# Kernel tuning notes

Measured on AMD Instinct MI355X. Metric: run time of the kernel, lower is better.

## Reference

```python
import jax, jax.numpy as jnp
import numpy as np

E = 512   # embed_size
H = 512   # hidden_size
V = 32000 # vocab_size
B = 32
P = 196   # num_pixels
T = 32    # seq_len


def setup_inputs() -> dict:
    key = jax.random.key(0)
    ks = jax.random.split(key, 16)
    s = 0.02
    return {
        "features": jax.random.normal(ks[0], (B, P, E), dtype=jnp.float32),
        "captions": jax.random.randint(ks[1], (B, T), 0, V),
        "embed_W": jax.random.normal(ks[2], (V, E), dtype=jnp.float32) * s,
        "attn_W": jax.random.normal(ks[3], (H, E + H), dtype=jnp.float32) * s,
        "attn_b": jnp.zeros((H,), dtype=jnp.float32),
        "v_w": jax.random.normal(ks[4], (H,), dtype=jnp.float32) * s,
        "W_ih": jax.random.normal(ks[5], (4 * H, 2 * E), dtype=jnp.float32) * s,
        "W_hh": jax.random.normal(ks[6], (4 * H, H), dtype=jnp.float32) * s,
        "b_ih": jnp.zeros((4 * H,), dtype=jnp.float32),
        "b_hh": jnp.zeros((4 * H,), dtype=jnp.float32),
        "lin_W": jax.random.normal(ks[7], (V, H), dtype=jnp.float32) * s,
        "lin_b": jnp.zeros((V,), dtype=jnp.float32),
        "inith_W": jax.random.normal(ks[8], (H, E), dtype=jnp.float32) * s,
        "inith_b": jnp.zeros((H,), dtype=jnp.float32),
        "initc_W": jax.random.normal(ks[9], (H, E), dtype=jnp.float32) * s,
        "initc_b": jnp.zeros((H,), dtype=jnp.float32),
    }


def _decode(features, captions, embed_W, attn_W, attn_b, v_w,
            W_ih, W_hh, b_ih, b_hh, lin_W, lin_b,
            inith_W, inith_b, initc_W, initc_b):
    mean_feat = features.mean(axis=1)                       # [B,E]
    h0 = mean_feat @ inith_W.T + inith_b                    # [B,H]
    c0 = mean_feat @ initc_W.T + initc_b                    # [B,H]
    emb = embed_W[captions]                                  # [B,T,E]

    # split attention weight: attn(cat(features, hidden)) = feat@Wf.T + h@Wh.T + b
    Wf = attn_W[:, :E]                                       # [H,E]
    Wh = attn_W[:, E:]                                       # [H,H]
    # features are constant across timesteps: project once
    feat_proj = jnp.einsum('bpe,he->bph', features, Wf)      # [B,P,H]

    def step(carry, x_t):
        h, c = carry
        # Bahdanau attention
        energy = jnp.tanh(feat_proj + (h @ Wh.T)[:, None, :] + attn_b)  # [B,P,H]
        scores = jnp.einsum('bph,h->bp', energy, v_w)                    # [B,P]
        alpha = jax.nn.softmax(scores, axis=1)
        context = jnp.einsum('bp,bpe->be', alpha, features)              # [B,E]
        # LSTM cell (PyTorch gate order i,f,g,o)
        x = jnp.concatenate([x_t, context], axis=-1)                     # [B,2E]
        gates = x @ W_ih.T + b_ih + h @ W_hh.T + b_hh                    # [B,4H]
        i, f, g, o = jnp.split(gates, 4, axis=-1)
        c_new = jax.nn.sigmoid(f) * c + jax.nn.sigmoid(i) * jnp.tanh(g)
        h_new = jax.nn.sigmoid(o) * jnp.tanh(c_new)
        logits = h_new @ lin_W.T + lin_b                                 # [B,V]
        return (h_new, c_new), logits

    xs = jnp.transpose(emb, (1, 0, 2))                        # [T,B,E]
    _, outs = jax.lax.scan(step, (h0, c0), xs)                # [T,B,V]
    return jnp.transpose(outs, (1, 0, 2))                     # [B,T,V]


def reference(features, captions, embed_W, attn_W, attn_b, v_w,
              W_ih, W_hh, b_ih, b_hh, lin_W, lin_b,
              inith_W, inith_b, initc_W, initc_b):
    return _decode(features, captions, embed_W, attn_W, attn_b, v_w,
                   W_ih, W_hh, b_ih, b_hh, lin_W, lin_b,
                   inith_W, inith_b, initc_W, initc_b)
```

## Files before the change

kernel.cpp:

```cpp
#include <hip/hip_runtime.h>

#define E 512
#define H 512
#define V 32000
#define B 32
#define P 196
#define T 32
#define NB 256
#define NT 512

typedef __attribute__((ext_vector_type(8))) short s8v;
typedef __attribute__((ext_vector_type(4))) float f4v;

__device__ __forceinline__ float bf16_to_f(unsigned short u){
  return __uint_as_float(((unsigned)u) << 16);
}
__device__ __forceinline__ unsigned short f_to_bf16(float f){
  unsigned u = __float_as_uint(f);
  u += 0x7FFFu + ((u >> 16) & 1u);
  return (unsigned short)(u >> 16);
}
__device__ __forceinline__ float fast_tanh(float x){
  float e = __expf(2.0f*x);
  return 1.0f - 2.0f/(e + 1.0f);
}
__device__ __forceinline__ float sigmoidf_(float x){
  return 1.0f/(1.0f + __expf(-x));
}
__device__ __forceinline__ void load_lds16(const unsigned short* g, unsigned short* l){
  __builtin_amdgcn_global_load_lds(
      (const __attribute__((address_space(1))) void*)g,
      (__attribute__((address_space(3))) void*)l, 16, 0, 0);
}
__device__ __forceinline__ float dot4(float4 a, float4 b){
  return a.x*b.x + a.y*b.y + a.z*b.z + a.w*b.w;
}

#define AT_SCOPE __HIP_MEMORY_SCOPE_AGENT
__device__ __forceinline__ void cohstore(float* p, float v){
  __hip_atomic_store(p, v, __ATOMIC_RELAXED, AT_SCOPE);
}
__device__ __forceinline__ unsigned cohldu(const unsigned* p){
  return __hip_atomic_load(p, __ATOMIC_RELAXED, AT_SCOPE);
}
__device__ __forceinline__ void cohstu(unsigned* p, unsigned v){
  __hip_atomic_store(p, v, __ATOMIC_RELAXED, AT_SCOPE);
}

__device__ __forceinline__ void bar_arrive(unsigned* my, unsigned gen){
  __syncthreads();
  if (threadIdx.x == 0) cohstu(my, gen);
}
__device__ __forceinline__ void bar_wait(const unsigned* base, unsigned gen){
  if (threadIdx.x < 64){
    for (;;){
      unsigned mn = 0xffffffffu;
      for (int i = (int)threadIdx.x; i < 8; i += 64){
        unsigned v = cohldu(base + i);
        mn = v < mn ? v : mn;
      }
      #pragma unroll
      for (int off = 32; off; off >>= 1){
        unsigned o2 = (unsigned)__shfl_xor((int)mn, off);
        mn = o2 < mn ? o2 : mn;
      }
      if (mn >= gen) break;
      __builtin_amdgcn_s_sleep(1);
    }
    __builtin_amdgcn_sched_barrier(0);
  }
  __syncthreads();
}

__global__ void split_kernel(const float* __restrict__ src, int src_ld, int src_coff,
                             int rows,
                             unsigned short* __restrict__ dhi, unsigned short* __restrict__ dlo,
                             int dst_ld, int dst_coff)
{
  int n = rows << 9;
  for (int i = blockIdx.x*blockDim.x + threadIdx.x; i < n; i += gridDim.x*blockDim.x){
    int r = i >> 9, c = i & 511;
    float x = src[(size_t)r*src_ld + src_coff + c];
    unsigned short h = f_to_bf16(x);
    dhi[(size_t)r*dst_ld + dst_coff + c] = h;
    if (dlo) dlo[(size_t)r*dst_ld + dst_coff + c] = f_to_bf16(x - bf16_to_f(h));
  }
}

__global__ void embed_kernel(const int* __restrict__ caps, const float* __restrict__ embW,
                             unsigned short* __restrict__ ehi, unsigned short* __restrict__ elo)
{
  int row = blockIdx.x;
  int cap = caps[row];
  const float* s = embW + (size_t)cap*E;
  for (int e = threadIdx.x; e < E; e += blockDim.x){
    float x = s[e];
    unsigned short h = f_to_bf16(x);
    ehi[(size_t)row*E + e] = h;
    elo[(size_t)row*E + e] = f_to_bf16(x - bf16_to_f(h));
  }
}

__global__ __launch_bounds__(512) void prep_kernel(
    const float* __restrict__ feats,
    const float* __restrict__ inith_W, const float* __restrict__ inith_b,
    const float* __restrict__ initc_W, const float* __restrict__ initc_b,
    float* __restrict__ hgrp, float* __restrict__ c_state)
{
  __shared__ float mf[E];
  const int b = blockIdx.x, tid = threadIdx.x;
  const float* fb = feats + (size_t)b*P*E + tid;
  float s = 0.f;
  for (int p = 0; p < P; ++p) s += fb[(size_t)p*E];
  mf[tid] = s * (1.0f/196.0f);
  __syncthreads();
  const float* wh = inith_W + (size_t)tid*E;
  const float* wc = initc_W + (size_t)tid*E;
  float h0 = inith_b[tid], c0 = initc_b[tid];
  #pragma unroll 4
  for (int e = 0; e < E; e += 4){
    float4 a4 = *(const float4*)(wh + e);
    float4 b4 = *(const float4*)(wc + e);
    float4 m4 = *(const float4*)(mf + e);
    h0 += dot4(a4, m4);
    c0 += dot4(b4, m4);
  }
  hgrp[(size_t)b*512 + tid] = h0;
  c_state[b*512 + tid] = c0;
}

__global__ __launch_bounds__(256) void transpose_wh_kernel(
    const float* __restrict__ attn_W, float* __restrict__ WhT)
{
  __shared__ float tile[64][65];
  const int jt = blockIdx.x & 7, kt = blockIdx.x >> 3;
  const int tx = threadIdx.x & 63, ty = threadIdx.x >> 6;
  for (int r = ty; r < 64; r += 4)
    tile[r][tx] = attn_W[(size_t)(jt*64 + r)*(E+H) + E + kt*64 + tx];
  __syncthreads();
  for (int r = ty; r < 64; r += 4)
    WhT[(size_t)(kt*64 + r)*512 + jt*64 + tx] = tile[tx][r];
}

__global__ __launch_bounds__(256) void pack_whh_kernel(
    const float* __restrict__ Whh, float* __restrict__ Wpackh)
{
  __shared__ float tile[64][65];
  const int sub = blockIdx.x & 7, cg = (blockIdx.x >> 3) & 3, kg = blockIdx.x >> 5;
  const int tx = threadIdx.x & 63, ty = threadIdx.x >> 6;
  const int kbase = kg*64;
  for (int cl = ty; cl < 64; cl += 4){
    const int c = cg*64 + cl;
    const int gcol = (c >> 6)*512 + sub*64 + (c & 63);
    tile[cl][tx] = Whh[(size_t)gcol*512 + kbase + tx];
  }
  __syncthreads();
  for (int kk = ty; kk < 64; kk += 4)
    Wpackh[((size_t)sub*512 + kbase + kk)*256 + cg*64 + tx] = tile[tx][kk];
}

__global__ __launch_bounds__(256) void gemm_bt_kernel(
    const unsigned short* __restrict__ A0, const unsigned short* __restrict__ A1,
    const unsigned short* __restrict__ A2,
    const unsigned short* __restrict__ B0, const unsigned short* __restrict__ B1,
    const unsigned short* __restrict__ B2,
    float* __restrict__ Cc, const float* __restrict__ bias,
    int N, int K, int npasses, int mt, int swz)
{
  __shared__ __align__(16) unsigned short Al[128*32];
  __shared__ __align__(16) unsigned short Bl[128*32];
  const int tid = threadIdx.x;
  const int wid = tid >> 6, l = tid & 63;
  int f = blockIdx.x;
  if (swz) f = (f & 7)*((int)gridDim.x >> 3) + (f >> 3);
  const int m0 = (f % mt)*128, n0 = (f / mt)*128;
  const int wr = wid >> 1, wc = wid & 1;

  f4v acc[4][4];
  #pragma unroll
  for (int i = 0; i < 4; ++i)
    #pragma unroll
    for (int j = 0; j < 4; ++j) acc[i][j] = (f4v){0.f,0.f,0.f,0.f};

  const int s0 = tid, s1 = tid + 256;
  const int r0 = s0 >> 2, g0 = (s0 & 3) ^ ((r0 >> 1) & 3);
  const int r1 = s1 >> 2, g1 = (s1 & 3) ^ ((r1 >> 1) & 3);
  const int la = l & 15, ch = l >> 4;

  for (int pass = 0; pass < npasses; ++pass){
    const unsigned short* Ap = pass == 0 ? A0 : (pass == 1 ? A1 : A2);
    const unsigned short* Bp = pass == 0 ? B0 : (pass == 1 ? B1 : B2);
    for (int k0 = 0; k0 < K; k0 += 32){
      __syncthreads();
      load_lds16(Ap + (size_t)(m0 + r0)*K + k0 + g0*8, Al + s0*8);
      load_lds16(Ap + (size_t)(m0 + r1)*K + k0 + g1*8, Al + s1*8);
      load_lds16(Bp + (size_t)(n0 + r0)*K + k0 + g0*8, Bl + s0*8);
      load_lds16(Bp + (size_t)(n0 + r1)*K + k0 + g1*8, Bl + s1*8);
      __syncthreads();
      s8v av[4], bv[4];
      #pragma unroll
      for (int mi = 0; mi < 4; ++mi){
        int row = wr*64 + mi*16 + la;
        int cs = ch ^ ((row >> 1) & 3);
        av[mi] = *(const s8v*)(Al + (row*4 + cs)*8);
      }
      #pragma unroll
      for (int ni = 0; ni < 4; ++ni){
        int row = wc*64 + ni*16 + la;
        int cs = ch ^ ((row >> 1) & 3);
        bv[ni] = *(const s8v*)(Bl + (row*4 + cs)*8);
      }
      #pragma unroll
      for (int mi = 0; mi < 4; ++mi)
        #pragma unroll
        for (int ni = 0; ni < 4; ++ni)
          acc[mi][ni] = __builtin_amdgcn_mfma_f32_16x16x32_bf16(av[mi], bv[ni], acc[mi][ni], 0, 0, 0);
    }
  }
  #pragma unroll
  for (int mi = 0; mi < 4; ++mi){
    int row = m0 + wr*64 + mi*16 + (l >> 4)*4;
    #pragma unroll
    for (int ni = 0; ni < 4; ++ni){
      int col = n0 + wc*64 + ni*16 + (l & 15);
      float bb = bias ? bias[col] : 0.0f;
      #pragma unroll
      for (int r = 0; r < 4; ++r)
        Cc[(size_t)(row + r)*N + col] = acc[mi][ni][r] + bb;
    }
  }
}

__global__ __launch_bounds__(512, 1) void loop_kernel(
    const float* __restrict__ feat_proj,
    const float* __restrict__ WhT, const float* __restrict__ attn_b,
    const float* __restrict__ v_w, const float* __restrict__ Wpackh,
    const float* __restrict__ FW, const float* __restrict__ gates_emb,
    const float* __restrict__ b_ih, const float* __restrict__ b_hh,
    float* __restrict__ hgrp,
    const float* __restrict__ c_init,
    float* __restrict__ sps,
    unsigned short* __restrict__ hall_h, unsigned short* __restrict__ hall_l,
    unsigned* __restrict__ fm1, unsigned* __restrict__ fm3)
{
  __shared__ float hs[512];
  __shared__ float hwl[64];
  __shared__ float partA[8][72];
  __shared__ float aux[256];
  __shared__ float biasl[256];
  __shared__ float red[512];
  __shared__ float smx, sinv;

  const int blk = blockIdx.x, tid = threadIdx.x;
  const int b = blk >> 3, sub = blk & 7;
  const int gbase = blk & ~7;
  const int l = tid & 63, wv = tid >> 6;

  float wreg[64];
  #pragma unroll
  for (int kk = 0; kk < 64; ++kk)
    wreg[kk] = WhT[(size_t)(wv*64 + kk)*512 + sub*64 + l];
  float fpreg[25];
  #pragma unroll
  for (int i = 0; i < 25; ++i){
    const int p = wv + i*8;
    fpreg[i] = (p < P) ? feat_proj[((size_t)b*P + p)*512 + sub*64 + l] : 0.f;
  }
  for (int c = tid; c < 256; c += NT){
    const int gcol = (c >> 6)*512 + sub*64 + (c & 63);
    biasl[c] = b_ih[gcol] + b_hh[gcol];
  }
  const float vl = v_w[sub*64 + l];
  const float ab = (tid < 64) ? attn_b[sub*64 + tid] : 0.f;
  float c_reg = 0.f;
  if (tid < 64) c_reg = c_init[b*512 + sub*64 + tid];

  const int dc = tid & 255;
  const int kh = tid >> 8;
  const int gcol_d = (dc >> 6)*512 + sub*64 + (dc & 63);
  const float* wp_h = Wpackh + ((size_t)sub*512 + kh*256)*256 + dc;
  __syncthreads();

  for (int t = 0; t < T; ++t){
    const unsigned gen = (unsigned)(t + 1);

    float gepre[4];
    if (tid < 64){
      const float* ge = gates_emb + ((size_t)b*T + t)*2048;
      #pragma unroll
      for (int g = 0; g < 4; ++g) gepre[g] = ge[g*512 + sub*64 + tid];
    }

    hs[tid] = hgrp[((size_t)t*B + b)*512 + tid];
    __syncthreads();
    {
      const float* hk = hs + wv*64;
      float a = 0.f;
      #pragma unroll
      for (int kk = 0; kk < 64; ++kk) a += hk[kk] * wreg[kk];
      partA[wv][l] = a;
    }
    __syncthreads();
    if (tid < 64){
      float s = ab;
      #pragma unroll
      for (int k = 0; k < 8; ++k) s += partA[k][tid];
      hwl[tid] = s;
    }
    __syncthreads();

    {
      const float hj = hwl[l];
      float* spw = sps + (size_t)(t*B + b)*1600 + sub;
      #pragma unroll
      for (int i = 0; i < 25; ++i){
        const int p = wv + i*8;
        if (p >= P) break;
        float e2 = vl * fast_tanh(fpreg[i] + hj);
        #pragma unroll
        for (int off = 32; off; off >>= 1) e2 += __shfl_xor(e2, off);
        if (l == 0) cohstore(spw + p*8, e2);
      }
    }
    bar_arrive(fm1 + blk, gen);

    float acch0 = 0.f, acch1 = 0.f, acch2 = 0.f, acch3 = 0.f;
    {
      const float* hk = hs + kh*256;
      #pragma unroll 8
      for (int k = 0; k < 256; k += 4){
        acch0 += wp_h[(size_t)(k+0)*256] * hk[k+0];
        acch1 += wp_h[(size_t)(k+1)*256] * hk[k+1];
        acch2 += wp_h[(size_t)(k+2)*256] * hk[k+2];
        acch3 += wp_h[(size_t)(k+3)*256] * hk[k+3];
      }
    }
    bar_wait(fm1 + gbase, gen);

    {
      float sc_v = -1e30f;
      if (tid < P){
        const float* sp = sps + (size_t)(t*B + b)*1600 + tid*8;
        float4 q0 = *(const float4*)sp, q1 = *(const float4*)(sp + 4);
        sc_v = (q0.x + q0.y + q0.z + q0.w) + (q1.x + q1.y + q1.z + q1.w);
      }
      if (tid < 256) aux[tid] = sc_v;
      __syncthreads();
      if (tid < 64){
        float m = -1e30f;
        #pragma unroll
        for (int i = 0; i < 4; ++i) m = fmaxf(m, aux[tid + i*64]);
        #pragma unroll
        for (int off = 32; off; off >>= 1) m = fmaxf(m, __shfl_xor(m, off));
        if (tid == 0) smx = m;
      }
      __syncthreads();
      float al = (tid < P) ? __expf(sc_v - smx) : 0.f;
      if (tid < 256) aux[tid] = al;
      __syncthreads();
      if (tid < 64){
        float s = 0.f;
        #pragma unroll
        for (int i = 0; i < 4; ++i) s += aux[tid + i*64];
        #pragma unroll
        for (int off = 32; off; off >>= 1) s += __shfl_xor(s, off);
        if (tid == 0) sinv = 1.0f/s;
      }
      __syncthreads();
    }

    float accc = 0.f;
    {
      const float* fwb = FW + ((size_t)b*P + kh*98)*2048 + gcol_d;
      const float* ax = aux + kh*98;
      #pragma unroll 7
      for (int i = 0; i < 98; ++i)
        accc += ax[i] * fwb[(size_t)i*2048];
    }
    red[dc*2 + kh] = ((acch0 + acch1) + (acch2 + acch3)) + accc*sinv;
    __syncthreads();

    if (tid < 64){
      float gv[4];
      #pragma unroll
      for (int g = 0; g < 4; ++g){
        const int c = g*64 + tid;
        gv[g] = red[c*2] + red[c*2 + 1] + biasl[c] + gepre[g];
      }
      const float i_ = sigmoidf_(gv[0]);
      const float f_ = sigmoidf_(gv[1]);
      const float g_ = fast_tanh(gv[2]);
      const float o_ = sigmoidf_(gv[3]);
      const int j = sub*64 + tid;
      const float c_new = f_*c_reg + i_*g_;
      const float h_new = o_*fast_tanh(c_new);
      c_reg = c_new;
      cohstore(hgrp + ((size_t)(t+1)*B + b)*512 + j, h_new);
      const unsigned short hh = f_to_bf16(h_new);
      aux[tid] = __uint_as_float(((unsigned)hh << 16) |
                 (unsigned)f_to_bf16(h_new - bf16_to_f(hh)));
    }
    bar_arrive(fm3 + blk, gen);
    if (tid < 64){
      const unsigned pk = __float_as_uint(aux[tid]);
      const int j = sub*64 + tid;
      hall_h[((size_t)b*T + t)*512 + j] = (unsigned short)(pk >> 16);
      hall_l[((size_t)b*T + t)*512 + j] = (unsigned short)(pk & 0xffffu);
    }
    bar_wait(fm3 + gbase, gen);
  }
}

extern "C" void kernel_launch(void* const* d_in, const int* in_sizes, int n_in,
                              void* d_out, int out_size, void* d_ws, size_t ws_size,
                              hipStream_t stream)
{
  (void)in_sizes; (void)n_in; (void)out_size;
  const float* features = (const float*)d_in[0];
  const int*   captions = (const int*)d_in[1];
  const float* embed_W  = (const float*)d_in[2];
  const float* attn_W   = (const float*)d_in[3];
  const float* attn_b   = (const float*)d_in[4];
  const float* v_w      = (const float*)d_in[5];
  const float* W_ih     = (const float*)d_in[6];
  const float* W_hh     = (const float*)d_in[7];
  const float* b_ih     = (const float*)d_in[8];
  const float* b_hh     = (const float*)d_in[9];
  const float* lin_W    = (const float*)d_in[10];
  const float* lin_b    = (const float*)d_in[11];
  const float* inith_W  = (const float*)d_in[12];
  const float* inith_b  = (const float*)d_in[13];
  const float* initc_W  = (const float*)d_in[14];
  const float* initc_b  = (const float*)d_in[15];

  char* o = (char*)d_out;
  unsigned short* feat_hi   = (unsigned short*)o; o += (size_t)(B*P)*E*2;
  unsigned short* feat_lo   = (unsigned short*)o; o += (size_t)(B*P)*E*2;
  unsigned short* Wf_bf     = (unsigned short*)o; o += (size_t)H*E*2;
  float*          feat_proj = (float*)o;          o += (size_t)(B*P)*H*4;
  unsigned short* emb_hi    = (unsigned short*)o; o += (size_t)(B*T)*E*2;
  unsigned short* emb_lo    = (unsigned short*)o; o += (size_t)(B*T)*E*2;
  unsigned short* Wihe_hi   = (unsigned short*)o; o += (size_t)2048*512*2;
  unsigned short* Wihe_lo   = (unsigned short*)o; o += (size_t)2048*512*2;
  unsigned short* Wihc_hi   = (unsigned short*)o; o += (size_t)2048*512*2;
  unsigned short* Wihc_lo   = (unsigned short*)o; o += (size_t)2048*512*2;
  float*          gates_emb = (float*)o;          o += (size_t)(B*T)*2048*4;
  float*          Wpackh    = (float*)o;          o += (size_t)8*512*256*4;
  float*          FW        = (float*)o;          o += (size_t)(B*P)*2048*4;

  const size_t SZ_LIN  = (size_t)V*H*2;
  const size_t SZ_HALL = (size_t)(B*T)*H*2;
  const size_t SZ_HG   = (size_t)(T+1)*B*512*4;
  const size_t SZ_SPS  = (size_t)T*B*200*8*4;
  const size_t SZ_ST   = (size_t)B*H*4;
  const size_t SZ_WHT  = (size_t)H*H*4;
  const size_t SZ_FLG  = 4096;
  const size_t need_wo = SZ_LIN + 2*SZ_HALL + SZ_HG + SZ_SPS + SZ_ST + SZ_WHT + SZ_FLG;
  const bool three = (ws_size >= need_wo + SZ_LIN);

  char* w = (char*)d_ws;
  unsigned short* lin_hi  = (unsigned short*)w; w += SZ_LIN;
  unsigned short* lin_lo  = (unsigned short*)w; if (three) w += SZ_LIN;
  unsigned short* hall_hi = (unsigned short*)w; w += SZ_HALL;
  unsigned short* hall_lo = (unsigned short*)w; w += SZ_HALL;
  float*          hgrp    = (float*)w;          w += SZ_HG;
  float*          sps     = (float*)w;          w += SZ_SPS;
  float*          c_state = (float*)w;          w += SZ_ST;
  float*          WhT_ws  = (float*)w;          w += SZ_WHT;
  unsigned*       flags   = (unsigned*)w;       w += SZ_FLG;
  unsigned* fm1 = flags;
  unsigned* fm3 = flags + 256;

  split_kernel<<<2048, 256, 0, stream>>>(features, E, 0, B*P, feat_hi, feat_lo, E, 0);
  split_kernel<<<256, 256, 0, stream>>>(attn_W, E+H, 0, H, Wf_bf, nullptr, E, 0);
  split_kernel<<<2048, 256, 0, stream>>>(lin_W, 512, 0, V, lin_hi, three ? lin_lo : nullptr, 512, 0);
  split_kernel<<<1024, 256, 0, stream>>>(W_ih, 1024, 0, 2048, Wihe_hi, Wihe_lo, 512, 0);
  split_kernel<<<1024, 256, 0, stream>>>(W_ih, 1024, 512, 2048, Wihc_hi, Wihc_lo, 512, 0);
  embed_kernel<<<B*T, 256, 0, stream>>>(captions, embed_W, emb_hi, emb_lo);
  prep_kernel<<<B, 512, 0, stream>>>(features, inith_W, inith_b, initc_W, initc_b,
                                     hgrp, c_state);
  transpose_wh_kernel<<<64, 256, 0, stream>>>(attn_W, WhT_ws);
  pack_whh_kernel<<<256, 256, 0, stream>>>(W_hh, Wpackh);
  hipMemsetAsync(flags, 0, SZ_FLG, stream);

  gemm_bt_kernel<<<(B*P/128)*(E/128), 256, 0, stream>>>(
      feat_hi, feat_hi, feat_hi, Wf_bf, Wf_bf, Wf_bf,
      feat_proj, nullptr, E, E, 1, B*P/128, 0);
  gemm_bt_kernel<<<(B*T/128)*(2048/128), 256, 0, stream>>>(
      emb_hi, emb_lo, emb_hi, Wihe_hi, Wihe_hi, Wihe_lo,
      gates_emb, nullptr, 2048, 512, 3, B*T/128, 1);
  gemm_bt_kernel<<<(B*P/128)*(2048/128), 256, 0, stream>>>(
      feat_hi, feat_lo, feat_hi, Wihc_hi, Wihc_hi, Wihc_lo,
      FW, nullptr, 2048, 512, 3, B*P/128, 1);

  loop_kernel<<<NB, NT, 0, stream>>>(
      feat_proj, WhT_ws, attn_b, v_w, Wpackh, FW, gates_emb, b_ih, b_hh,
      hgrp, c_state, sps, hall_hi, hall_lo, fm1, fm3);

  gemm_bt_kernel<<<(V/128)*(B*T/128), 256, 0, stream>>>(
      hall_hi, hall_lo, hall_hi, lin_hi, lin_hi, three ? lin_lo : lin_hi,
      (float*)d_out, lin_b, V, H, three ? 3 : 2, B*T/128, 1);
}
```

Before: 1.061 ms.

## Store W_hh pack in bf16 and remap blocks so subs interleave across batches

The packed recurrent weight W_hh used in the per-step LSTM gate dot products is now stored as bf16 instead of fp32, halving the bytes streamed each timestep. Block-to-(batch,sub) mapping changes from b=blk>>3 to b=blk&31 so that blocks sharing the same weight slice are adjacent, which may improve L2 locality across CUs/XCDs. Flag indices are recomputed to match the new mapping. This lowers the precision of the h@W_hh product, which could affect accuracy.

After: 1.029 ms. -2.9%, faster.

```diff
diff --git a/kernel.cpp b/kernel.cpp
--- a/kernel.cpp
+++ b/kernel.cpp
@@ -143,7 +143,7 @@
 }
 
 __global__ __launch_bounds__(256) void pack_whh_kernel(
-    const float* __restrict__ Whh, float* __restrict__ Wpackh)
+    const float* __restrict__ Whh, unsigned short* __restrict__ Wpackh)
 {
   __shared__ float tile[64][65];
   const int sub = blockIdx.x & 7, cg = (blockIdx.x >> 3) & 3, kg = blockIdx.x >> 5;
@@ -156,7 +156,7 @@
   }
   __syncthreads();
   for (int kk = ty; kk < 64; kk += 4)
-    Wpackh[((size_t)sub*512 + kbase + kk)*256 + cg*64 + tx] = tile[tx][kk];
+    Wpackh[((size_t)sub*512 + kbase + kk)*256 + cg*64 + tx] = f_to_bf16(tile[tx][kk]);
 }
 
 __global__ __launch_bounds__(256) void gemm_bt_kernel(
@@ -234,7 +234,7 @@
 __global__ __launch_bounds__(512, 1) void loop_kernel(
     const float* __restrict__ feat_proj,
     const float* __restrict__ WhT, const float* __restrict__ attn_b,
-    const float* __restrict__ v_w, const float* __restrict__ Wpackh,
+    const float* __restrict__ v_w, const unsigned short* __restrict__ Wpackh,
     const float* __restrict__ FW, const float* __restrict__ gates_emb,
     const float* __restrict__ b_ih, const float* __restrict__ b_hh,
     float* __restrict__ hgrp,
@@ -252,8 +252,7 @@
   __shared__ float smx, sinv;
 
   const int blk = blockIdx.x, tid = threadIdx.x;
-  const int b = blk >> 3, sub = blk & 7;
-  const int gbase = blk & ~7;
+  const int b = blk & 31, sub = blk >> 5;
   const int l = tid & 63, wv = tid >> 6;
 
   float wreg[64];
@@ -278,7 +277,8 @@
   const int dc = tid & 255;
   const int kh = tid >> 8;
   const int gcol_d = (dc >> 6)*512 + sub*64 + (dc & 63);
-  const float* wp_h = Wpackh + ((size_t)sub*512 + kh*256)*256 + dc;
+  const unsigned short* wp_h = Wpackh + ((size_t)sub*512 + kh*256)*256 + dc;
+  const float* fw_th = FW + ((size_t)b*P + kh*98)*2048 + gcol_d;
   __syncthreads();
 
   for (int t = 0; t < T; ++t){
@@ -322,20 +322,20 @@
         if (l == 0) cohstore(spw + p*8, e2);
       }
     }
-    bar_arrive(fm1 + blk, gen);
+    bar_arrive(fm1 + b*8 + sub, gen);
 
     float acch0 = 0.f, acch1 = 0.f, acch2 = 0.f, acch3 = 0.f;
     {
       const float* hk = hs + kh*256;
       #pragma unroll 8
       for (int k = 0; k < 256; k += 4){
-        acch0 += wp_h[(size_t)(k+0)*256] * hk[k+0];
-        acch1 += wp_h[(size_t)(k+1)*256] * hk[k+1];
-        acch2 += wp_h[(size_t)(k+2)*256] * hk[k+2];
-        acch3 += wp_h[(size_t)(k+3)*256] * hk[k+3];
-      }
-    }
-    bar_wait(fm1 + gbase, gen);
+        acch0 += bf16_to_f(wp_h[(size_t)(k+0)*256]) * hk[k+0];
+        acch1 += bf16_to_f(wp_h[(size_t)(k+1)*256]) * hk[k+1];
+        acch2 += bf16_to_f(wp_h[(size_t)(k+2)*256]) * hk[k+2];
+        acch3 += bf16_to_f(wp_h[(size_t)(k+3)*256]) * hk[k+3];
+      }
+    }
+    bar_wait(fm1 + b*8, gen);
 
     {
       float sc_v = -1e30f;
@@ -371,11 +371,10 @@
 
     float accc = 0.f;
     {
-      const float* fwb = FW + ((size_t)b*P + kh*98)*2048 + gcol_d;
       const float* ax = aux + kh*98;
       #pragma unroll 7
       for (int i = 0; i < 98; ++i)
-        accc += ax[i] * fwb[(size_t)i*2048];
+        accc += ax[i] * fw_th[(size_t)i*2048];
     }
     red[dc*2 + kh] = ((acch0 + acch1) + (acch2 + acch3)) + accc*sinv;
     __syncthreads();
@@ -400,14 +399,14 @@
       aux[tid] = __uint_as_float(((unsigned)hh << 16) |
                  (unsigned)f_to_bf16(h_new - bf16_to_f(hh)));
     }
-    bar_arrive(fm3 + blk, gen);
+    bar_arrive(fm3 + b*8 + sub, gen);
     if (tid < 64){
       const unsigned pk = __float_as_uint(aux[tid]);
       const int j = sub*64 + tid;
       hall_h[((size_t)b*T + t)*512 + j] = (unsigned short)(pk >> 16);
       hall_l[((size_t)b*T + t)*512 + j] = (unsigned short)(pk & 0xffffu);
     }
-    bar_wait(fm3 + gbase, gen);
+    bar_wait(fm3 + b*8, gen);
   }
 }
 
@@ -445,7 +444,7 @@
   unsigned short* Wihc_hi   = (unsigned short*)o; o += (size_t)2048*512*2;
   unsigned short* Wihc_lo   = (unsigned short*)o; o += (size_t)2048*512*2;
   float*          gates_emb = (float*)o;          o += (size_t)(B*T)*2048*4;
-  float*          Wpackh    = (float*)o;          o += (size_t)8*512*256*4;
+  unsigned short* Wpackh    = (unsigned short*)o; o += (size_t)8*512*256*2;
   float*          FW        = (float*)o;          o += (size_t)(B*P)*2048*4;
 
   const size_t SZ_LIN  = (size_t)V*H*2;
```
